# Optimization experiments

Hardware: AMD Instinct MI355X
Metric: run time of the kernel (lower is better)

## Reference

```python
import jax, jax.numpy as jnp
import numpy as np


def setup_inputs() -> dict:
    key = jax.random.key(0)
    ks = jax.random.split(key, 6)
    B, N, d = 8, 2048, 64
    h = jax.random.normal(ks[0], (B, N, d), dtype=jnp.float32)
    adj = jax.random.randint(ks[1], (B, N, N), 0, 2, dtype=jnp.int32)
    h_root = jax.random.normal(ks[2], (B, N), dtype=jnp.float32)
    weight = jax.random.normal(ks[3], (d, d), dtype=jnp.float32) * (1.0 / np.sqrt(d))
    a1 = jax.random.normal(ks[4], (d, 1), dtype=jnp.float32) * (1.0 / np.sqrt(d))
    a2 = jax.random.normal(ks[5], (d, 1), dtype=jnp.float32) * (1.0 / np.sqrt(d))
    return {"h": h, "adj": adj, "h_root": h_root, "weight": weight, "a1": a1, "a2": a2}


def reference(h, adj, h_root, weight, a1, a2):
    h0 = h
    hw = jax.nn.relu(jnp.matmul(h, weight))          # (B,N,d)
    t1 = jnp.matmul(hw, a1)                          # (B,N,1)
    t2 = jnp.matmul(hw, a2)                          # (B,N,1)
    # e[b,i,j] = relu(t1[b,i] + t2[b,j])  (broadcast, same as repeat/view in torch)
    e = jax.nn.relu(t1 + jnp.swapaxes(t2, -1, -2))   # (B,N,N)
    # FAITHFUL to source bug: pos0 = -9e15 * zeros_like(adj) == 0, so
    # non-edges get logit 0 (not -inf) before softmax.
    e = jnp.where(adj > 0, e, jnp.zeros_like(e))
    attention = jax.nn.softmax(e, axis=-1)           # (B,N,N)
    embedding = jnp.matmul(attention, hw)            # (B,N,d)
    # assign = h_root[:,:,None] @ ones(B,1,d) -> h_root broadcast over d;
    # assign > 0  <=>  h_root > 0 since ones are positive.
    assign = h_root[:, :, None] * jnp.ones((1, 1, hw.shape[-1]), dtype=hw.dtype)
    embedding = jnp.where(assign > 0, embedding, h0)
    return embedding
```

## Files before the change

### kernel.cpp

```cpp
#include <hip/hip_runtime.h>
#include <hip/hip_bf16.h>

#define BATCH 8
#define NN    2048
#define DD    64
#define BN    (BATCH * NN)
#define MWORDS 66

typedef __attribute__((ext_vector_type(8))) short bf16x8;
typedef __attribute__((ext_vector_type(4))) float f32x4;

static __device__ __forceinline__ unsigned f2bf_pk(float lo, float hi) {
  unsigned ul = __float_as_uint(lo);
  unsigned uh = __float_as_uint(hi);
  ul = (ul + 0x7fffu + ((ul >> 16) & 1u)) >> 16;
  uh = (uh + 0x7fffu + ((uh >> 16) & 1u)) & 0xffff0000u;
  return ul | uh;
}

__global__ __launch_bounds__(256) void k1_hw_t1_t2(
    const float* __restrict__ h, const float* __restrict__ W,
    const float* __restrict__ a1, const float* __restrict__ a2,
    unsigned short* __restrict__ hwT, float* __restrict__ t1, float* __restrict__ t2) {
  __shared__ float ht[64 * 36];
  __shared__ float Ws[64 * 64];
  __shared__ unsigned short bt[64 * 40];

  const int t  = threadIdx.x;
  const int r0 = blockIdx.x * 32;

#pragma unroll
  for (int r = 0; r < 4; ++r) {
    int f = t + 256 * r;
    reinterpret_cast<float4*>(Ws)[f] = reinterpret_cast<const float4*>(W)[f];
  }
#pragma unroll
  for (int r = 0; r < 2; ++r) {
    int f = t + 256 * r;
    int i = f >> 4, j4 = f & 15;
    float4 v = reinterpret_cast<const float4*>(h + (size_t)(r0 + i) * DD)[j4];
    ht[(4 * j4 + 0) * 36 + i] = v.x;
    ht[(4 * j4 + 1) * 36 + i] = v.y;
    ht[(4 * j4 + 2) * 36 + i] = v.z;
    ht[(4 * j4 + 3) * 36 + i] = v.w;
  }
  __syncthreads();

  const int trow = t >> 4, kcol = t & 15;
  float4 acc0 = make_float4(0.f, 0.f, 0.f, 0.f);
  float4 acc1 = make_float4(0.f, 0.f, 0.f, 0.f);

#pragma unroll 8
  for (int j = 0; j < 64; ++j) {
    float2 hv = *reinterpret_cast<const float2*>(&ht[j * 36 + 2 * trow]);
    float4 wv = reinterpret_cast<const float4*>(Ws)[j * 16 + kcol];
    acc0.x = fmaf(hv.x, wv.x, acc0.x); acc0.y = fmaf(hv.x, wv.y, acc0.y);
    acc0.z = fmaf(hv.x, wv.z, acc0.z); acc0.w = fmaf(hv.x, wv.w, acc0.w);
    acc1.x = fmaf(hv.y, wv.x, acc1.x); acc1.y = fmaf(hv.y, wv.y, acc1.y);
    acc1.z = fmaf(hv.y, wv.z, acc1.z); acc1.w = fmaf(hv.y, wv.w, acc1.w);
  }

  acc0.x = fmaxf(acc0.x, 0.f); acc0.y = fmaxf(acc0.y, 0.f);
  acc0.z = fmaxf(acc0.z, 0.f); acc0.w = fmaxf(acc0.w, 0.f);
  acc1.x = fmaxf(acc1.x, 0.f); acc1.y = fmaxf(acc1.y, 0.f);
  acc1.z = fmaxf(acc1.z, 0.f); acc1.w = fmaxf(acc1.w, 0.f);

  float4 a1v = reinterpret_cast<const float4*>(a1)[kcol];
  float4 a2v = reinterpret_cast<const float4*>(a2)[kcol];
  float s1_0 = acc0.x * a1v.x + acc0.y * a1v.y + acc0.z * a1v.z + acc0.w * a1v.w;
  float s1_1 = acc1.x * a1v.x + acc1.y * a1v.y + acc1.z * a1v.z + acc1.w * a1v.w;
  float s2_0 = acc0.x * a2v.x + acc0.y * a2v.y + acc0.z * a2v.z + acc0.w * a2v.w;
  float s2_1 = acc1.x * a2v.x + acc1.y * a2v.y + acc1.z * a2v.z + acc1.w * a2v.w;
#pragma unroll
  for (int mm = 1; mm <= 8; mm <<= 1) {
    s1_0 += __shfl_xor(s1_0, mm, 64);
    s1_1 += __shfl_xor(s1_1, mm, 64);
    s2_0 += __shfl_xor(s2_0, mm, 64);
    s2_1 += __shfl_xor(s2_1, mm, 64);
  }
  {
    int row = r0 + 2 * trow;
    if (kcol == 0) {
      t1[row] = s1_0; t1[row + 1] = s1_1;
      t2[row] = s2_0; t2[row + 1] = s2_1;
    }
  }

  {
    const float* a0 = &acc0.x;
    const float* a1p = &acc1.x;
#pragma unroll
    for (int c = 0; c < 4; ++c) {
      int k = 4 * kcol + c;
      *reinterpret_cast<unsigned*>(&bt[k * 40 + 2 * trow]) = f2bf_pk(a0[c], a1p[c]);
    }
  }
  __syncthreads();
  {
    int k = t >> 2, jp = t & 3;
    int g = k >> 4, n = k & 15;
    int bb = r0 >> 11;
    int jb = r0 & (NN - 1);
    int ks = jb >> 5;
    size_t base = ((((size_t)bb * (NN / 32) + ks) * 4 + g) * 64 + (jp * 16 + n)) * 8;
    *reinterpret_cast<int4*>(hwT + base) = *reinterpret_cast<const int4*>(&bt[k * 40 + jp * 8]);
  }
}

__global__ __launch_bounds__(256, 4) void k2_attn(
    const unsigned short* __restrict__ hwT, const int* __restrict__ adj,
    const float* __restrict__ t1, const float* __restrict__ t2,
    const float* __restrict__ h, const float* __restrict__ h_root,
    float* __restrict__ out) {
  __shared__ unsigned maskS[16 * MWORDS];
  __shared__ float t2s[NN];
  __shared__ float os[4][16][68];
  __shared__ float denos[4][16];

  const int t    = threadIdx.x;
  const int b    = blockIdx.x >> 7;
  const int i0   = (blockIdx.x & 127) * 16;
  const int w    = t >> 6;
  const int lane = t & 63;
  const int m    = lane & 15;
  const int quad = lane >> 4;

#pragma unroll
  for (int r = 0; r < 2; ++r)
    reinterpret_cast<float4*>(t2s)[t + 256 * r] =
        reinterpret_cast<const float4*>(t2 + b * NN)[t + 256 * r];

  const int rowbase = b * NN + i0;

#pragma unroll 1
  for (int rr = 0; rr < 4; ++rr) {
    const int row = w * 4 + rr;
    const bool active = h_root[rowbase + row] > 0.f;
    if (active) {
      const int* ap = adj + (size_t)(rowbase + row) * NN + lane;
#pragma unroll 1
      for (int sb = 0; sb < 2; ++sb) {
        int v[16];
#pragma unroll
        for (int s = 0; s < 16; ++s) v[s] = ap[(sb * 16 + s) * 64];
#pragma unroll
        for (int s = 0; s < 16; ++s) {
          unsigned long long bal = __ballot(v[s] > 0);
          if (lane == 0)
            *reinterpret_cast<unsigned long long*>(
                &maskS[row * MWORDS + (sb * 16 + s) * 2]) = bal;
        }
      }
    } else {
      maskS[row * MWORDS + lane] = 0u;
    }
  }
  __syncthreads();

  const float t1v = t1[rowbase + m];
  const int ks0 = w * 16;

  f32x4 acc[4];
#pragma unroll
  for (int g = 0; g < 4; ++g) acc[g] = (f32x4){0.f, 0.f, 0.f, 0.f};
  float den = 0.f;

  unsigned mcur = maskS[m * MWORDS + ks0];

#pragma unroll 1
  for (int kk = 0; kk < 16; ++kk) {
    const int ks = ks0 + kk;
    unsigned mnext = 0;
    if (kk + 1 < 16) mnext = maskS[m * MWORDS + ks + 1];

    const unsigned short* bp =
        hwT + ((((size_t)b * (NN / 32) + ks) * 4) * 64 + lane) * 8;
    bf16x8 B0 = *reinterpret_cast<const bf16x8*>(bp);
    bf16x8 B1 = *reinterpret_cast<const bf16x8*>(bp + 512);
    bf16x8 B2 = *reinterpret_cast<const bf16x8*>(bp + 1024);
    bf16x8 B3 = *reinterpret_cast<const bf16x8*>(bp + 1536);

    const float* t2p = &t2s[ks * 32 + quad * 8];
    float4 e0 = *reinterpret_cast<const float4*>(t2p);
    float4 e1 = *reinterpret_cast<const float4*>(t2p + 4);

    const unsigned mm8 = mcur >> (quad * 8);
    float p0 = (mm8 & 1u)   ? __expf(fmaxf(t1v + e0.x, 0.f)) : 1.f;
    float p1 = (mm8 & 2u)   ? __expf(fmaxf(t1v + e0.y, 0.f)) : 1.f;
    float p2 = (mm8 & 4u)   ? __expf(fmaxf(t1v + e0.z, 0.f)) : 1.f;
    float p3 = (mm8 & 8u)   ? __expf(fmaxf(t1v + e0.w, 0.f)) : 1.f;
    float p4 = (mm8 & 16u)  ? __expf(fmaxf(t1v + e1.x, 0.f)) : 1.f;
    float p5 = (mm8 & 32u)  ? __expf(fmaxf(t1v + e1.y, 0.f)) : 1.f;
    float p6 = (mm8 & 64u)  ? __expf(fmaxf(t1v + e1.z, 0.f)) : 1.f;
    float p7 = (mm8 & 128u) ? __expf(fmaxf(t1v + e1.w, 0.f)) : 1.f;
    den += ((p0 + p1) + (p2 + p3)) + ((p4 + p5) + (p6 + p7));

    union { bf16x8 v; unsigned u[4]; } Af;
    Af.u[0] = f2bf_pk(p0, p1); Af.u[1] = f2bf_pk(p2, p3);
    Af.u[2] = f2bf_pk(p4, p5); Af.u[3] = f2bf_pk(p6, p7);

    acc[0] = __builtin_amdgcn_mfma_f32_16x16x32_bf16(Af.v, B0, acc[0], 0, 0, 0);
    acc[1] = __builtin_amdgcn_mfma_f32_16x16x32_bf16(Af.v, B1, acc[1], 0, 0, 0);
    acc[2] = __builtin_amdgcn_mfma_f32_16x16x32_bf16(Af.v, B2, acc[2], 0, 0, 0);
    acc[3] = __builtin_amdgcn_mfma_f32_16x16x32_bf16(Af.v, B3, acc[3], 0, 0, 0);

    mcur = mnext;
  }

  den += __shfl_xor(den, 16, 64);
  den += __shfl_xor(den, 32, 64);
  if (quad == 0) denos[w][m] = den;

#pragma unroll
  for (int g = 0; g < 4; ++g)
#pragma unroll
    for (int r = 0; r < 4; ++r)
      os[w][quad * 4 + r][g * 16 + m] = acc[g][r];
  __syncthreads();

  {
    const int i = t >> 4, k4 = t & 15;
    float4 a = make_float4(0.f, 0.f, 0.f, 0.f);
    float d = 0.f;
#pragma unroll
    for (int ww = 0; ww < 4; ++ww) {
      float4 p = *reinterpret_cast<const float4*>(&os[ww][i][k4 * 4]);
      a.x += p.x; a.y += p.y; a.z += p.z; a.w += p.w;
      d += denos[ww][i];
    }
    const size_t row = (size_t)rowbase + i;
    float4 res;
    if (h_root[row] > 0.f) {
      const float inv = 1.f / d;
      res.x = a.x * inv; res.y = a.y * inv; res.z = a.z * inv; res.w = a.w * inv;
    } else {
      res = reinterpret_cast<const float4*>(h + row * DD)[k4];
    }
    reinterpret_cast<float4*>(out + row * DD)[k4] = res;
  }
}

extern "C" void kernel_launch(void* const* d_in, const int* in_sizes, int n_in,
                              void* d_out, int out_size, void* d_ws, size_t ws_size,
                              hipStream_t stream) {
  const float* h      = (const float*)d_in[0];
  const int*   adj    = (const int*)d_in[1];
  const float* h_root = (const float*)d_in[2];
  const float* W      = (const float*)d_in[3];
  const float* a1     = (const float*)d_in[4];
  const float* a2     = (const float*)d_in[5];
  float* out = (float*)d_out;

  unsigned short* hwT = (unsigned short*)d_ws;
  float* t1 = (float*)(hwT + (size_t)BN * DD);
  float* t2 = t1 + BN;

  k1_hw_t1_t2<<<BN / 32, 256, 0, stream>>>(h, W, a1, a2, hwT, t1, t2);
  k2_attn<<<BATCH * (NN / 16), 256, 0, stream>>>(hwT, adj, t1, t2, h, h_root, out);
}
```

Measured before the change: 210.2 us.

## Factor exp(relu(t1+t2)) into max(e^t1·e^t2,1) and interleave batches across blocks

Precomputes exp(t1) and exp(t2) in the first kernel so the attention kernel replaces a per-pair exp with a multiply and max against 1, using exp(relu(x)) = max(exp(x), 1). It also remaps block indices so consecutive blocks cover different batches, and widens the mask row stride from 66 to 68 words. The exp factorisation can overflow or lose precision for large logits. The attention kernel is likely dominated by streaming the int32 adjacency matrix, so the ALU savings may matter little.

```diff
diff --git a/kernel.cpp b/kernel.cpp
--- a/kernel.cpp
+++ b/kernel.cpp
@@ -5,7 +5,7 @@
 #define NN    2048
 #define DD    64
 #define BN    (BATCH * NN)
-#define MWORDS 66
+#define MWORDS 68
 
 typedef __attribute__((ext_vector_type(8))) short bf16x8;
 typedef __attribute__((ext_vector_type(4))) float f32x4;
@@ -21,7 +21,7 @@
 __global__ __launch_bounds__(256) void k1_hw_t1_t2(
     const float* __restrict__ h, const float* __restrict__ W,
     const float* __restrict__ a1, const float* __restrict__ a2,
-    unsigned short* __restrict__ hwT, float* __restrict__ t1, float* __restrict__ t2) {
+    unsigned short* __restrict__ hwT, float* __restrict__ e1, float* __restrict__ e2) {
   __shared__ float ht[64 * 36];
   __shared__ float Ws[64 * 64];
   __shared__ unsigned short bt[64 * 40];
@@ -81,8 +81,8 @@
   {
     int row = r0 + 2 * trow;
     if (kcol == 0) {
-      t1[row] = s1_0; t1[row + 1] = s1_1;
-      t2[row] = s2_0; t2[row + 1] = s2_1;
+      e1[row] = __expf(s1_0); e1[row + 1] = __expf(s1_1);
+      e2[row] = __expf(s2_0); e2[row + 1] = __expf(s2_1);
     }
   }
 
@@ -109,28 +109,27 @@
 
 __global__ __launch_bounds__(256, 4) void k2_attn(
     const unsigned short* __restrict__ hwT, const int* __restrict__ adj,
-    const float* __restrict__ t1, const float* __restrict__ t2,
+    const float* __restrict__ e1, const float* __restrict__ e2,
     const float* __restrict__ h, const float* __restrict__ h_root,
     float* __restrict__ out) {
   __shared__ unsigned maskS[16 * MWORDS];
-  __shared__ float t2s[NN];
+  __shared__ float e2s[NN];
   __shared__ float os[4][16][68];
   __shared__ float denos[4][16];
 
   const int t    = threadIdx.x;
-  const int b    = blockIdx.x >> 7;
-  const int i0   = (blockIdx.x & 127) * 16;
+  const int b    = blockIdx.x & 7;
+  const int i0   = (blockIdx.x >> 3) * 16;
   const int w    = t >> 6;
   const int lane = t & 63;
   const int m    = lane & 15;
   const int quad = lane >> 4;
+  const int rowbase = b * NN + i0;
 
 #pragma unroll
   for (int r = 0; r < 2; ++r)
-    reinterpret_cast<float4*>(t2s)[t + 256 * r] =
-        reinterpret_cast<const float4*>(t2 + b * NN)[t + 256 * r];
-
-  const int rowbase = b * NN + i0;
+    reinterpret_cast<float4*>(e2s)[t + 256 * r] =
+        reinterpret_cast<const float4*>(e2 + b * NN)[t + 256 * r];
 
 #pragma unroll 1
   for (int rr = 0; rr < 4; ++rr) {
@@ -157,7 +156,7 @@
   }
   __syncthreads();
 
-  const float t1v = t1[rowbase + m];
+  const float E1v = e1[rowbase + m];
   const int ks0 = w * 16;
 
   f32x4 acc[4];
@@ -180,19 +179,19 @@
     bf16x8 B2 = *reinterpret_cast<const bf16x8*>(bp + 1024);
     bf16x8 B3 = *reinterpret_cast<const bf16x8*>(bp + 1536);
 
-    const float* t2p = &t2s[ks * 32 + quad * 8];
-    float4 e0 = *reinterpret_cast<const float4*>(t2p);
-    float4 e1 = *reinterpret_cast<const float4*>(t2p + 4);
+    const float* e2p = &e2s[ks * 32 + quad * 8];
+    float4 g0 = *reinterpret_cast<const float4*>(e2p);
+    float4 g1 = *reinterpret_cast<const float4*>(e2p + 4);
 
     const unsigned mm8 = mcur >> (quad * 8);
-    float p0 = (mm8 & 1u)   ? __expf(fmaxf(t1v + e0.x, 0.f)) : 1.f;
-    float p1 = (mm8 & 2u)   ? __expf(fmaxf(t1v + e0.y, 0.f)) : 1.f;
-    float p2 = (mm8 & 4u)   ? __expf(fmaxf(t1v + e0.z, 0.f)) : 1.f;
-    float p3 = (mm8 & 8u)   ? __expf(fmaxf(t1v + e0.w, 0.f)) : 1.f;
-    float p4 = (mm8 & 16u)  ? __expf(fmaxf(t1v + e1.x, 0.f)) : 1.f;
-    float p5 = (mm8 & 32u)  ? __expf(fmaxf(t1v + e1.y, 0.f)) : 1.f;
-    float p6 = (mm8 & 64u)  ? __expf(fmaxf(t1v + e1.z, 0.f)) : 1.f;
-    float p7 = (mm8 & 128u) ? __expf(fmaxf(t1v + e1.w, 0.f)) : 1.f;
+    float p0 = (mm8 & 1u)   ? fmaxf(E1v * g0.x, 1.f) : 1.f;
+    float p1 = (mm8 & 2u)   ? fmaxf(E1v * g0.y, 1.f) : 1.f;
+    float p2 = (mm8 & 4u)   ? fmaxf(E1v * g0.z, 1.f) : 1.f;
+    float p3 = (mm8 & 8u)   ? fmaxf(E1v * g0.w, 1.f) : 1.f;
+    float p4 = (mm8 & 16u)  ? fmaxf(E1v * g1.x, 1.f) : 1.f;
+    float p5 = (mm8 & 32u)  ? fmaxf(E1v * g1.y, 1.f) : 1.f;
+    float p6 = (mm8 & 64u)  ? fmaxf(E1v * g1.z, 1.f) : 1.f;
+    float p7 = (mm8 & 128u) ? fmaxf(E1v * g1.w, 1.f) : 1.f;
     den += ((p0 + p1) + (p2 + p3)) + ((p4 + p5) + (p6 + p7));
 
     union { bf16x8 v; unsigned u[4]; } Af;
@@ -252,9 +251,9 @@
   float* out = (float*)d_out;
 
   unsigned short* hwT = (unsigned short*)d_ws;
-  float* t1 = (float*)(hwT + (size_t)BN * DD);
-  float* t2 = t1 + BN;
-
-  k1_hw_t1_t2<<<BN / 32, 256, 0, stream>>>(h, W, a1, a2, hwT, t1, t2);
-  k2_attn<<<BATCH * (NN / 16), 256, 0, stream>>>(hwT, adj, t1, t2, h, h_root, out);
-}
+  float* e1 = (float*)(hwT + (size_t)BN * DD);
+  float* e2 = e1 + BN;
+
+  k1_hw_t1_t2<<<BN / 32, 256, 0, stream>>>(h, W, a1, a2, hwT, e1, e2);
+  k2_attn<<<BATCH * (NN / 16), 256, 0, stream>>>(hwT, adj, e1, e2, h, h_root, out);
+}
```

Result: no change. 208.3 us, median of 2 (-0.9%).
